# Optimization experiments

Measured on AMD Instinct MI355X. Metric: run time of the kernel, lower is better.

The kernel has to match this reference:

```python
import jax, jax.numpy as jnp
import numpy as np

Z, P, CIN, COUT, E, HID = 4, 512, 32, 32, 65536, 128

def setup_inputs() -> dict:
    key = jax.random.key(0)
    ks = jax.random.split(key, 8)
    return {
        "features": jax.random.normal(ks[0], (Z, P, CIN), dtype=jnp.float32),
        "edge_vec": jax.random.normal(ks[1], (E, 3), dtype=jnp.float32),
        "W1": jax.random.normal(ks[2], (4, HID), dtype=jnp.float32) * 0.5,
        "b1": jax.random.normal(ks[3], (HID,), dtype=jnp.float32) * 0.1,
        "W2": jax.random.normal(ks[4], (HID, COUT * CIN), dtype=jnp.float32) * (1.0 / np.sqrt(HID)),
        "edge_batch": jax.random.randint(ks[5], (E,), 0, Z),
        "edge_a": jax.random.randint(ks[6], (E,), 0, P),
        "edge_b": jax.random.randint(ks[7], (E,), 0, P),
        "n_norm": 1,
    }

def reference(features, edge_vec, W1, b1, W2, edge_batch, edge_a, edge_b, n_norm):
    Zb, Pn, Cin = features.shape
    # zero near-degenerate radii (matches radius[norm < 1e-10] = 0)
    r = jnp.linalg.norm(edge_vec, axis=-1, keepdims=True)  # [E,1]
    vec = jnp.where(r < 1e-10, jnp.zeros_like(edge_vec), edge_vec)
    rn = jnp.where(r < 1e-10, jnp.zeros_like(r), r)
    # per-edge kernel: MLP(vec, |vec|) -> [E, c_out, c_in]
    x = jnp.concatenate([vec, rn], axis=-1)               # [E,4]
    h = jax.nn.relu(x @ W1 + b1)                          # [E,HID]
    Cout = W2.shape[1] // Cin
    k = (h @ W2).reshape(-1, Cout, Cin)                   # [E,co,ci]
    # gather neighbor features, per-edge matvec, scatter-add to centers
    f_b = features[edge_batch, edge_b]                    # [E,ci]
    msg = jnp.einsum('eij,ej->ei', k, f_b)                # [E,co]
    seg = edge_batch * Pn + edge_a
    out = jax.ops.segment_sum(msg, seg, num_segments=Zb * Pn)
    out = out.reshape(Zb, Pn, Cout)
    return out / jnp.sqrt(jnp.asarray(n_norm, dtype=features.dtype))
```

## Files before the change

kernel.cpp:

```cpp
#include <hip/hip_runtime.h>

#define ZBATCH 4
#define PN     512
#define CINC   32
#define COUTC  32
#define EN     65536
#define HIDN   128
#define NNODE  (ZBATCH*PN)
#define CAP    128
#define HP     64
#define WFW    (HP*COUTC)

using hvec2 = decltype(__builtin_amdgcn_cvt_pkrtz(0.f, 0.f));

static __device__ __forceinline__ unsigned packh2(float a, float b) {
  hvec2 h = __builtin_amdgcn_cvt_pkrtz(a, b);
  unsigned u;
  __builtin_memcpy(&u, &h, 4);
  return u;
}

static __device__ __forceinline__ float dot2acc(unsigned hu, unsigned wu,
                                                float acc) {
  hvec2 a, b;
  __builtin_memcpy(&a, &hu, 4);
  __builtin_memcpy(&b, &wu, 4);
#if __has_builtin(__builtin_amdgcn_fdot2)
  return __builtin_amdgcn_fdot2(a, b, acc, false);
#else
  acc = fmaf((float)a.x, (float)b.x, acc);
  return fmaf((float)a.y, (float)b.y, acc);
#endif
}

__global__ __launch_bounds__(256) void k1_bin_wf(
    const float* __restrict__ F, const float* __restrict__ W2,
    unsigned* __restrict__ Wf, const int* __restrict__ eb,
    const int* __restrict__ ea, const int* __restrict__ ebn,
    int* __restrict__ cnt_src, int* __restrict__ cnt_dst,
    int* __restrict__ order_src, int* __restrict__ order_dst) {
  const int t = threadIdx.x;
  const int b = blockIdx.x;
  if (b < 256) {
    const int e = b * 256 + t;
    const int zb = eb[e];
    const int ns = zb * PN + ebn[e];
    const int nd = zb * PN + ea[e];
    const int p = atomicAdd(&cnt_src[ns], 1);
    if (p < CAP) order_src[ns * CAP + p] = e;
    const int q = atomicAdd(&cnt_dst[nd], 1);
    if (q < CAP) order_dst[nd * CAP + q] = e;
    return;
  }
  const int bb = b - 256;
  const int jt = bb & 7, ntile = bb >> 3;
  const int hp = t & 63;
  const int co = jt * 4 + (t >> 6);
  const float4* rA = (const float4*)(W2 + (size_t)(2 * hp) * (COUTC * CINC)
                                     + co * CINC);
  const float4* rB = (const float4*)(W2 + (size_t)(2 * hp + 1) * (COUTC * CINC)
                                     + co * CINC);
  float4 wa[8], wb[8];
#pragma unroll
  for (int q = 0; q < 8; ++q) { wa[q] = rA[q]; wb[q] = rB[q]; }
  const int n0 = ntile * 32;
  for (int n = 0; n < 32; ++n) {
    const float4* fr = (const float4*)(F + (size_t)(n0 + n) * CINC);
    float a0 = 0.f, a1 = 0.f, a2 = 0.f, a3 = 0.f;
    float c0 = 0.f, c1 = 0.f, c2 = 0.f, c3 = 0.f;
#pragma unroll
    for (int q = 0; q < 8; ++q) {
      const float4 f = fr[q];
      a0 = fmaf(f.x, wa[q].x, a0); a1 = fmaf(f.y, wa[q].y, a1);
      a2 = fmaf(f.z, wa[q].z, a2); a3 = fmaf(f.w, wa[q].w, a3);
      c0 = fmaf(f.x, wb[q].x, c0); c1 = fmaf(f.y, wb[q].y, c1);
      c2 = fmaf(f.z, wb[q].z, c2); c3 = fmaf(f.w, wb[q].w, c3);
    }
    Wf[(size_t)(n0 + n) * WFW + co * HP + hp] =
        packh2((a0 + a1) + (a2 + a3), (c0 + c1) + (c2 + c3));
  }
}

__global__ __launch_bounds__(256) void k2_msg(
    const float* __restrict__ evec, const float* __restrict__ W1,
    const float* __restrict__ b1, const unsigned* __restrict__ Wf,
    const int* __restrict__ cnt_src, const int* __restrict__ order_src,
    const int* __restrict__ nn, float* __restrict__ msg) {
  const int n = blockIdx.x;
  const int t = threadIdx.x;
  const int lane = t & 63, w = t >> 6;
  const int co = lane & 31, hh = lane >> 5;

  __shared__ int ords[CAP];
  __shared__ __align__(16) unsigned Hbuf[4][8][64];

  const int c0 = cnt_src[n];
  const int count = c0 < CAP ? c0 : CAP;
  if (count == 0) return;

  uint4 wfv[8];
  {
    const uint4* wp = (const uint4*)(Wf + (size_t)n * WFW + co * HP + hh * 32);
#pragma unroll
    for (int q = 0; q < 8; ++q) wfv[q] = wp[q];
  }
  if (t < count) ords[t] = order_src[(size_t)n * CAP + t];
  const int h0 = lane << 1;
  const float2 u0 = *(const float2*)(W1 + 0 * HIDN + h0);
  const float2 u1 = *(const float2*)(W1 + 1 * HIDN + h0);
  const float2 u2 = *(const float2*)(W1 + 2 * HIDN + h0);
  const float2 u3 = *(const float2*)(W1 + 3 * HIDN + h0);
  const float2 b2 = *(const float2*)(b1 + h0);
  const float scale = rsqrtf((float)nn[0]);
  __syncthreads();

  for (int base = w * 8; base < count; base += 32) {
    int e8[8]; float ex[8], ey[8], ez[8];
#pragma unroll
    for (int i = 0; i < 8; ++i) {
      const int idx = (base + i < count) ? (base + i) : (count - 1);
      e8[i] = ords[idx];
    }
#pragma unroll
    for (int i = 0; i < 8; ++i) {
      ex[i] = evec[3 * e8[i]];
      ey[i] = evec[3 * e8[i] + 1];
      ez[i] = evec[3 * e8[i] + 2];
    }
#pragma unroll
    for (int i = 0; i < 8; ++i) {
      const float r = sqrtf(ex[i] * ex[i] + ey[i] * ey[i] + ez[i] * ez[i]);
      const bool bad = (r < 1e-10f);
      const float y0 = bad ? 0.f : ex[i], y1 = bad ? 0.f : ey[i];
      const float y2 = bad ? 0.f : ez[i], y3 = bad ? 0.f : r;
      const float a0 = fmaf(y3, u3.x, fmaf(y2, u2.x,
                       fmaf(y1, u1.x, fmaf(y0, u0.x, b2.x))));
      const float a1 = fmaf(y3, u3.y, fmaf(y2, u2.y,
                       fmaf(y1, u1.y, fmaf(y0, u0.y, b2.y))));
      Hbuf[w][i][lane] = packh2(fmaxf(a0, 0.f), fmaxf(a1, 0.f));
    }
    __builtin_amdgcn_wave_barrier();
#pragma unroll
    for (int i = 0; i < 8; ++i) {
      const uint4* hp4 = (const uint4*)&Hbuf[w][i][hh * 32];
      float s0 = 0.f, s1 = 0.f, s2 = 0.f, s3 = 0.f;
#pragma unroll
      for (int q = 0; q < 8; ++q) {
        const uint4 hv = hp4[q];
        s0 = dot2acc(hv.x, wfv[q].x, s0);
        s1 = dot2acc(hv.y, wfv[q].y, s1);
        s2 = dot2acc(hv.z, wfv[q].z, s2);
        s3 = dot2acc(hv.w, wfv[q].w, s3);
      }
      float acc = (s0 + s1) + (s2 + s3);
      acc += __shfl_xor(acc, 32);
      if (hh == 0 && base + i < count)
        msg[(size_t)e8[i] * COUTC + co] = acc * scale;
    }
    __builtin_amdgcn_wave_barrier();
  }
}

__global__ __launch_bounds__(256) void k3_reduce(
    const float* __restrict__ msg, const int* __restrict__ cnt_dst,
    const int* __restrict__ order_dst, float* __restrict__ out) {
  const int t = threadIdx.x;
  const int lane = t & 63, w = t >> 6;
  const int co = lane & 31, hh = lane >> 5;
  const int n = blockIdx.x * 4 + w;
  __shared__ int idxs[4][CAP];
  const int c0 = cnt_dst[n];
  const int count = c0 < CAP ? c0 : CAP;
  for (int i = lane; i < count; i += 64)
    idxs[w][i] = order_dst[(size_t)n * CAP + i];
  __builtin_amdgcn_wave_barrier();
  float a0 = 0.f, a1 = 0.f, a2 = 0.f, a3 = 0.f;
  for (int g = hh * 4; g < count; g += 8) {
    const int i1 = g + 1, i2 = g + 2, i3 = g + 3;
    a0 += msg[(size_t)idxs[w][g] * COUTC + co];
    if (i1 < count) a1 += msg[(size_t)idxs[w][i1] * COUTC + co];
    if (i2 < count) a2 += msg[(size_t)idxs[w][i2] * COUTC + co];
    if (i3 < count) a3 += msg[(size_t)idxs[w][i3] * COUTC + co];
  }
  float acc = (a0 + a1) + (a2 + a3);
  acc += __shfl_xor(acc, 32);
  if (hh == 0) out[(size_t)n * COUTC + co] = acc;
}

extern "C" void kernel_launch(void* const* d_in, const int* in_sizes, int n_in,
                              void* d_out, int out_size, void* d_ws, size_t ws_size,
                              hipStream_t stream) {
  const float* features   = (const float*)d_in[0];
  const float* edge_vec   = (const float*)d_in[1];
  const float* W1         = (const float*)d_in[2];
  const float* b1         = (const float*)d_in[3];
  const float* W2         = (const float*)d_in[4];
  const int*   edge_batch = (const int*)d_in[5];
  const int*   edge_a     = (const int*)d_in[6];
  const int*   edge_b     = (const int*)d_in[7];
  const int*   n_norm     = (const int*)d_in[8];
  float* out = (float*)d_out;

  char* ws = (char*)d_ws;
  unsigned* Wf = (unsigned*)ws;
  float* msg = (float*)(ws + (size_t)NNODE * WFW * 4);
  int* ints = (int*)(ws + (size_t)NNODE * WFW * 4 + (size_t)EN * COUTC * 4);
  int* cnt_src   = ints;
  int* cnt_dst   = ints + NNODE;
  int* order_src = ints + 2 * NNODE;
  int* order_dst = order_src + NNODE * CAP;
  const size_t need = (size_t)NNODE * WFW * 4 + (size_t)EN * COUTC * 4
                    + (size_t)(2 * NNODE + 2 * NNODE * CAP) * 4;
  if (ws_size < need) return;

  (void)hipMemsetAsync(cnt_src, 0, 2 * NNODE * 4, stream);
  k1_bin_wf<<<256 + 512, 256, 0, stream>>>(features, W2, Wf, edge_batch,
                                           edge_a, edge_b, cnt_src, cnt_dst,
                                           order_src, order_dst);
  k2_msg<<<NNODE, 256, 0, stream>>>(edge_vec, W1, b1, Wf, cnt_src, order_src,
                                    n_norm, msg);
  k3_reduce<<<NNODE / 4, 256, 0, stream>>>(msg, cnt_dst, order_dst, out);
}
```

Before: 141.1 us.

## Map one wavefront per source node in k2 and prefetch next edge batch

The message kernel now gives each wavefront its own source node instead of splitting one node's edges across four waves of a block. Block-wide __syncthreads goes away and the launch grid shrinks by four. The edge vectors for the next batch of 8 edges are loaded before the current batch's dot products run, software-pipelining the gather latency. In exchange each wave now does all of a node's ~32 edges serially and needs more registers for the prefetch, and per-wave work becomes uneven across nodes.

```diff
diff --git a/kernel.cpp b/kernel.cpp
--- a/kernel.cpp
+++ b/kernel.cpp
@@ -86,25 +86,27 @@
     const float* __restrict__ b1, const unsigned* __restrict__ Wf,
     const int* __restrict__ cnt_src, const int* __restrict__ order_src,
     const int* __restrict__ nn, float* __restrict__ msg) {
-  const int n = blockIdx.x;
   const int t = threadIdx.x;
   const int lane = t & 63, w = t >> 6;
+  const int n = blockIdx.x * 4 + w;
   const int co = lane & 31, hh = lane >> 5;
 
-  __shared__ int ords[CAP];
+  __shared__ int ords[4][CAP];
   __shared__ __align__(16) unsigned Hbuf[4][8][64];
 
   const int c0 = cnt_src[n];
   const int count = c0 < CAP ? c0 : CAP;
   if (count == 0) return;
 
+  if (lane < count) ords[w][lane] = order_src[(size_t)n * CAP + lane];
+  if (lane + 64 < count) ords[w][lane + 64] = order_src[(size_t)n * CAP + lane + 64];
+
   uint4 wfv[8];
   {
     const uint4* wp = (const uint4*)(Wf + (size_t)n * WFW + co * HP + hh * 32);
 #pragma unroll
     for (int q = 0; q < 8; ++q) wfv[q] = wp[q];
   }
-  if (t < count) ords[t] = order_src[(size_t)n * CAP + t];
   const int h0 = lane << 1;
   const float2 u0 = *(const float2*)(W1 + 0 * HIDN + h0);
   const float2 u1 = *(const float2*)(W1 + 1 * HIDN + h0);
@@ -112,32 +114,46 @@
   const float2 u3 = *(const float2*)(W1 + 3 * HIDN + h0);
   const float2 b2 = *(const float2*)(b1 + h0);
   const float scale = rsqrtf((float)nn[0]);
-  __syncthreads();
-
-  for (int base = w * 8; base < count; base += 32) {
-    int e8[8]; float ex[8], ey[8], ez[8];
-#pragma unroll
-    for (int i = 0; i < 8; ++i) {
-      const int idx = (base + i < count) ? (base + i) : (count - 1);
-      e8[i] = ords[idx];
-    }
-#pragma unroll
-    for (int i = 0; i < 8; ++i) {
-      ex[i] = evec[3 * e8[i]];
-      ey[i] = evec[3 * e8[i] + 1];
-      ez[i] = evec[3 * e8[i] + 2];
-    }
-#pragma unroll
-    for (int i = 0; i < 8; ++i) {
-      const float r = sqrtf(ex[i] * ex[i] + ey[i] * ey[i] + ez[i] * ez[i]);
-      const bool bad = (r < 1e-10f);
+  __builtin_amdgcn_wave_barrier();
+
+  int e8[8]; float ex[8], ey[8], ez[8];
+#pragma unroll
+  for (int i = 0; i < 8; ++i) {
+    const int idx = (i < count) ? i : (count - 1);
+    e8[i] = ords[w][idx];
+  }
+#pragma unroll
+  for (int i = 0; i < 8; ++i) {
+    ex[i] = evec[3 * e8[i]];
+    ey[i] = evec[3 * e8[i] + 1];
+    ez[i] = evec[3 * e8[i] + 2];
+  }
+
+  for (int base = 0; base < count; base += 8) {
+#pragma unroll
+    for (int i = 0; i < 8; ++i) {
+      const float r2 = sqrtf(ex[i] * ex[i] + ey[i] * ey[i] + ez[i] * ez[i]);
+      const bool bad = (r2 < 1e-10f);
       const float y0 = bad ? 0.f : ex[i], y1 = bad ? 0.f : ey[i];
-      const float y2 = bad ? 0.f : ez[i], y3 = bad ? 0.f : r;
+      const float y2 = bad ? 0.f : ez[i], y3 = bad ? 0.f : r2;
       const float a0 = fmaf(y3, u3.x, fmaf(y2, u2.x,
                        fmaf(y1, u1.x, fmaf(y0, u0.x, b2.x))));
       const float a1 = fmaf(y3, u3.y, fmaf(y2, u2.y,
                        fmaf(y1, u1.y, fmaf(y0, u0.y, b2.y))));
       Hbuf[w][i][lane] = packh2(fmaxf(a0, 0.f), fmaxf(a1, 0.f));
+    }
+    int f8[8]; float fx[8], fy[8], fz[8];
+    const int nb = base + 8;
+#pragma unroll
+    for (int i = 0; i < 8; ++i) {
+      const int idx = (nb + i < count) ? (nb + i) : (count - 1);
+      f8[i] = ords[w][idx];
+    }
+#pragma unroll
+    for (int i = 0; i < 8; ++i) {
+      fx[i] = evec[3 * f8[i]];
+      fy[i] = evec[3 * f8[i] + 1];
+      fz[i] = evec[3 * f8[i] + 2];
     }
     __builtin_amdgcn_wave_barrier();
 #pragma unroll
@@ -158,6 +174,10 @@
         msg[(size_t)e8[i] * COUTC + co] = acc * scale;
     }
     __builtin_amdgcn_wave_barrier();
+#pragma unroll
+    for (int i = 0; i < 8; ++i) {
+      e8[i] = f8[i]; ex[i] = fx[i]; ey[i] = fy[i]; ez[i] = fz[i];
+    }
   }
 }
 
@@ -217,7 +237,7 @@
   k1_bin_wf<<<256 + 512, 256, 0, stream>>>(features, W2, Wf, edge_batch,
                                            edge_a, edge_b, cnt_src, cnt_dst,
                                            order_src, order_dst);
-  k2_msg<<<NNODE, 256, 0, stream>>>(edge_vec, W1, b1, Wf, cnt_src, order_src,
-                                    n_norm, msg);
+  k2_msg<<<NNODE / 4, 256, 0, stream>>>(edge_vec, W1, b1, Wf, cnt_src,
+                                        order_src, n_norm, msg);
   k3_reduce<<<NNODE / 4, 256, 0, stream>>>(msg, cnt_dst, order_dst, out);
 }
```

After: 144.3 us. 2.3% more time.

## Compute per-edge messages with MFMA f16 matrix ops, one node per wave

Applied to the files above, without the earlier changes.

Replaces the per-lane fdot2 dot products in the message kernel with 16x16x32 f16 MFMA instructions. The folded weight matrix Wf is re-laid out in k1 to match the MFMA B-operand fragment order, and hidden activations are staged in XOR-swizzled LDS for the A operand. Each wave now handles one source node, processing 16 edges per tile, and the grid shrinks by four. This aims to cut the VALU cost of the hidden-to-output contraction, at the price of padding partial tiles to 16 edges and doing scalar edge-vector loads per edge.

```diff
diff --git a/kernel.cpp b/kernel.cpp
--- a/kernel.cpp
+++ b/kernel.cpp
@@ -8,29 +8,17 @@
 #define HIDN   128
 #define NNODE  (ZBATCH*PN)
 #define CAP    128
-#define HP     64
-#define WFW    (HP*COUTC)
+#define WFW    2048
 
 using hvec2 = decltype(__builtin_amdgcn_cvt_pkrtz(0.f, 0.f));
+typedef __attribute__((ext_vector_type(8))) _Float16 f16x8;
+typedef __attribute__((ext_vector_type(4))) float f32x4;
 
 static __device__ __forceinline__ unsigned packh2(float a, float b) {
   hvec2 h = __builtin_amdgcn_cvt_pkrtz(a, b);
   unsigned u;
   __builtin_memcpy(&u, &h, 4);
   return u;
-}
-
-static __device__ __forceinline__ float dot2acc(unsigned hu, unsigned wu,
-                                                float acc) {
-  hvec2 a, b;
-  __builtin_memcpy(&a, &hu, 4);
-  __builtin_memcpy(&b, &wu, 4);
-#if __has_builtin(__builtin_amdgcn_fdot2)
-  return __builtin_amdgcn_fdot2(a, b, acc, false);
-#else
-  acc = fmaf((float)a.x, (float)b.x, acc);
-  return fmaf((float)a.y, (float)b.y, acc);
-#endif
 }
 
 __global__ __launch_bounds__(256) void k1_bin_wf(
@@ -56,6 +44,9 @@
   const int jt = bb & 7, ntile = bb >> 3;
   const int hp = t & 63;
   const int co = jt * 4 + (t >> 6);
+  const int ks = hp >> 4, g = (hp >> 2) & 3, j = hp & 3;
+  const int nt = co >> 4, col = co & 15;
+  const int flat = (ks * 2 + nt) * 256 + g * 64 + col * 4 + j;
   const float4* rA = (const float4*)(W2 + (size_t)(2 * hp) * (COUTC * CINC)
                                      + co * CINC);
   const float4* rB = (const float4*)(W2 + (size_t)(2 * hp + 1) * (COUTC * CINC)
@@ -76,7 +67,7 @@
       c0 = fmaf(f.x, wb[q].x, c0); c1 = fmaf(f.y, wb[q].y, c1);
       c2 = fmaf(f.z, wb[q].z, c2); c3 = fmaf(f.w, wb[q].w, c3);
     }
-    Wf[(size_t)(n0 + n) * WFW + co * HP + hp] =
+    Wf[(size_t)(n0 + n) * WFW + flat] =
         packh2((a0 + a1) + (a2 + a3), (c0 + c1) + (c2 + c3));
   }
 }
@@ -86,25 +77,31 @@
     const float* __restrict__ b1, const unsigned* __restrict__ Wf,
     const int* __restrict__ cnt_src, const int* __restrict__ order_src,
     const int* __restrict__ nn, float* __restrict__ msg) {
-  const int n = blockIdx.x;
   const int t = threadIdx.x;
   const int lane = t & 63, w = t >> 6;
-  const int co = lane & 31, hh = lane >> 5;
-
-  __shared__ int ords[CAP];
-  __shared__ __align__(16) unsigned Hbuf[4][8][64];
+  const int n = blockIdx.x * 4 + w;
+  const int col = lane & 15, g = lane >> 4;
+
+  __shared__ int ords[4][CAP];
+  __shared__ __align__(16) unsigned Hb[4][1024];
 
   const int c0 = cnt_src[n];
   const int count = c0 < CAP ? c0 : CAP;
   if (count == 0) return;
 
-  uint4 wfv[8];
+  if (lane < count) ords[w][lane] = order_src[(size_t)n * CAP + lane];
+  if (lane + 64 < count)
+    ords[w][lane + 64] = order_src[(size_t)n * CAP + lane + 64];
+
+  f16x8 bf[8];
   {
-    const uint4* wp = (const uint4*)(Wf + (size_t)n * WFW + co * HP + hh * 32);
-#pragma unroll
-    for (int q = 0; q < 8; ++q) wfv[q] = wp[q];
-  }
-  if (t < count) ords[t] = order_src[(size_t)n * CAP + t];
+    const unsigned* wfb = Wf + (size_t)n * WFW + g * 64 + col * 4;
+#pragma unroll
+    for (int q = 0; q < 8; ++q) {
+      const uint4 braw = *(const uint4*)(wfb + q * 256);
+      __builtin_memcpy(&bf[q], &braw, 16);
+    }
+  }
   const int h0 = lane << 1;
   const float2 u0 = *(const float2*)(W1 + 0 * HIDN + h0);
   const float2 u1 = *(const float2*)(W1 + 1 * HIDN + h0);
@@ -112,50 +109,52 @@
   const float2 u3 = *(const float2*)(W1 + 3 * HIDN + h0);
   const float2 b2 = *(const float2*)(b1 + h0);
   const float scale = rsqrtf((float)nn[0]);
-  __syncthreads();
-
-  for (int base = w * 8; base < count; base += 32) {
-    int e8[8]; float ex[8], ey[8], ez[8];
-#pragma unroll
-    for (int i = 0; i < 8; ++i) {
-      const int idx = (base + i < count) ? (base + i) : (count - 1);
-      e8[i] = ords[idx];
-    }
-#pragma unroll
-    for (int i = 0; i < 8; ++i) {
-      ex[i] = evec[3 * e8[i]];
-      ey[i] = evec[3 * e8[i] + 1];
-      ez[i] = evec[3 * e8[i] + 2];
-    }
-#pragma unroll
-    for (int i = 0; i < 8; ++i) {
-      const float r = sqrtf(ex[i] * ex[i] + ey[i] * ey[i] + ez[i] * ez[i]);
-      const bool bad = (r < 1e-10f);
-      const float y0 = bad ? 0.f : ex[i], y1 = bad ? 0.f : ey[i];
-      const float y2 = bad ? 0.f : ez[i], y3 = bad ? 0.f : r;
-      const float a0 = fmaf(y3, u3.x, fmaf(y2, u2.x,
-                       fmaf(y1, u1.x, fmaf(y0, u0.x, b2.x))));
-      const float a1 = fmaf(y3, u3.y, fmaf(y2, u2.y,
-                       fmaf(y1, u1.y, fmaf(y0, u0.y, b2.y))));
-      Hbuf[w][i][lane] = packh2(fmaxf(a0, 0.f), fmaxf(a1, 0.f));
+  __builtin_amdgcn_wave_barrier();
+
+  const int arow = col;
+  const unsigned axor = (unsigned)((arow & 7) << 2);
+
+  for (int base = 0; base < count; base += 16) {
+#pragma unroll
+    for (int i = 0; i < 16; ++i) {
+      unsigned word = 0;
+      if (base + i < count) {
+        const int e = __builtin_amdgcn_readfirstlane(ords[w][base + i]);
+        const float x0 = evec[3 * e], x1 = evec[3 * e + 1], x2 = evec[3 * e + 2];
+        const float r2 = sqrtf(x0 * x0 + x1 * x1 + x2 * x2);
+        const bool bad = (r2 < 1e-10f);
+        const float y0 = bad ? 0.f : x0, y1 = bad ? 0.f : x1;
+        const float y2 = bad ? 0.f : x2, y3 = bad ? 0.f : r2;
+        const float a0 = fmaf(y3, u3.x, fmaf(y2, u2.x,
+                         fmaf(y1, u1.x, fmaf(y0, u0.x, b2.x))));
+        const float a1 = fmaf(y3, u3.y, fmaf(y2, u2.y,
+                         fmaf(y1, u1.y, fmaf(y0, u0.y, b2.y))));
+        word = packh2(fmaxf(a0, 0.f), fmaxf(a1, 0.f));
+      }
+      Hb[w][(unsigned)(i * 64 + lane) ^ ((unsigned)(i & 7) << 2)] = word;
     }
     __builtin_amdgcn_wave_barrier();
-#pragma unroll
-    for (int i = 0; i < 8; ++i) {
-      const uint4* hp4 = (const uint4*)&Hbuf[w][i][hh * 32];
-      float s0 = 0.f, s1 = 0.f, s2 = 0.f, s3 = 0.f;
-#pragma unroll
-      for (int q = 0; q < 8; ++q) {
-        const uint4 hv = hp4[q];
-        s0 = dot2acc(hv.x, wfv[q].x, s0);
-        s1 = dot2acc(hv.y, wfv[q].y, s1);
-        s2 = dot2acc(hv.z, wfv[q].z, s2);
-        s3 = dot2acc(hv.w, wfv[q].w, s3);
+    f32x4 acc0 = {0.f, 0.f, 0.f, 0.f};
+    f32x4 acc1 = {0.f, 0.f, 0.f, 0.f};
+#pragma unroll
+    for (int ks = 0; ks < 4; ++ks) {
+      const unsigned aidx = ((unsigned)(arow * 64 + ks * 16 + g * 4)) ^ axor;
+      const uint4 araw = *(const uint4*)&Hb[w][aidx];
+      f16x8 af;
+      __builtin_memcpy(&af, &araw, 16);
+      acc0 = __builtin_amdgcn_mfma_f32_16x16x32_f16(af, bf[ks * 2 + 0], acc0, 0, 0, 0);
+      acc1 = __builtin_amdgcn_mfma_f32_16x16x32_f16(af, bf[ks * 2 + 1], acc1, 0, 0, 0);
+    }
+    __builtin_amdgcn_wave_barrier();
+#pragma unroll
+    for (int r = 0; r < 4; ++r) {
+      const int row = g * 4 + r;
+      const int gi = base + row;
+      if (gi < count) {
+        const int e = ords[w][gi];
+        msg[(size_t)e * COUTC + col]      = acc0[r] * scale;
+        msg[(size_t)e * COUTC + 16 + col] = acc1[r] * scale;
       }
-      float acc = (s0 + s1) + (s2 + s3);
-      acc += __shfl_xor(acc, 32);
-      if (hh == 0 && base + i < count)
-        msg[(size_t)e8[i] * COUTC + co] = acc * scale;
     }
     __builtin_amdgcn_wave_barrier();
   }
@@ -175,9 +174,9 @@
     idxs[w][i] = order_dst[(size_t)n * CAP + i];
   __builtin_amdgcn_wave_barrier();
   float a0 = 0.f, a1 = 0.f, a2 = 0.f, a3 = 0.f;
-  for (int g = hh * 4; g < count; g += 8) {
-    const int i1 = g + 1, i2 = g + 2, i3 = g + 3;
-    a0 += msg[(size_t)idxs[w][g] * COUTC + co];
+  for (int gq = hh * 4; gq < count; gq += 8) {
+    const int i1 = gq + 1, i2 = gq + 2, i3 = gq + 3;
+    a0 += msg[(size_t)idxs[w][gq] * COUTC + co];
     if (i1 < count) a1 += msg[(size_t)idxs[w][i1] * COUTC + co];
     if (i2 < count) a2 += msg[(size_t)idxs[w][i2] * COUTC + co];
     if (i3 < count) a3 += msg[(size_t)idxs[w][i3] * COUTC + co];
@@ -217,7 +216,7 @@
   k1_bin_wf<<<256 + 512, 256, 0, stream>>>(features, W2, Wf, edge_batch,
                                            edge_a, edge_b, cnt_src, cnt_dst,
                                            order_src, order_dst);
-  k2_msg<<<NNODE, 256, 0, stream>>>(edge_vec, W1, b1, Wf, cnt_src, order_src,
-                                    n_norm, msg);
+  k2_msg<<<NNODE / 4, 256, 0, stream>>>(edge_vec, W1, b1, Wf, cnt_src,
+                                        order_src, n_norm, msg);
   k3_reduce<<<NNODE / 4, 256, 0, stream>>>(msg, cnt_dst, order_dst, out);
 }
```

Result: no change. 143.1 us (+1.4%).
